# Performance work log

Measured on AMD Instinct MI355X. Metric: run time of the kernel, lower is better.

The kernel has to match this reference:

```python
import jax, jax.numpy as jnp
import numpy as np

NUM_WINDOWS = 162   # icosphere order-2 windows
NUM_HEADS = 8

def layernorm(x, g, b, eps=1e-5):
    m = jnp.mean(x, axis=-1, keepdims=True)
    v = jnp.var(x, axis=-1, keepdims=True)
    return (x - m) * jax.lax.rsqrt(v + eps) * g + b

def setup_inputs() -> dict:
    key = jax.random.key(0)
    ks = jax.random.split(key, 16)
    B, N, C = 1, 41472, 512
    H, hid = NUM_HEADS, 4 * 512
    s = 0.02
    # window assignment: 162 windows x 256 vertices, shuffled (gather-based partition)
    rng = np.random.default_rng(0)
    wid = np.repeat(np.arange(NUM_WINDOWS), N // NUM_WINDOWS)
    rng.shuffle(wid)
    return {
        "x": jax.random.normal(ks[0], (B, N, C), jnp.float32),
        "mesh": jax.random.normal(ks[1], (N, 3), jnp.float32),
        "ln1_g": jnp.ones((C,), jnp.float32),
        "ln1_b": jnp.zeros((C,), jnp.float32),
        "qkv_w": jax.random.normal(ks[2], (C, 3 * C), jnp.float32) * s,
        "qkv_b": jnp.zeros((3 * C,), jnp.float32),
        "rel_bias": jax.random.normal(ks[3], (H, 1, 1), jnp.float32) * s,
        "proj_w": jax.random.normal(ks[4], (C, C), jnp.float32) * s,
        "proj_b": jnp.zeros((C,), jnp.float32),
        "ln2_g": jnp.ones((C,), jnp.float32),
        "ln2_b": jnp.zeros((C,), jnp.float32),
        "ffn_w1": jax.random.normal(ks[5], (C, hid), jnp.float32) * s,
        "ffn_b1": jnp.zeros((hid,), jnp.float32),
        "ffn_w2": jax.random.normal(ks[6], (hid, C), jnp.float32) * s,
        "ffn_b2": jnp.zeros((C,), jnp.float32),
        "window_ids": jnp.asarray(wid, dtype=jnp.int32),
    }

def reference(x, mesh, ln1_g, ln1_b, qkv_w, qkv_b, rel_bias, proj_w, proj_b,
              ln2_g, ln2_b, ffn_w1, ffn_b1, ffn_w2, ffn_b2, window_ids):
    B, N, C = x.shape
    H = NUM_HEADS
    hd = C // H
    ws = N // NUM_WINDOWS
    # --- gather-based window partition ---
    idx = jnp.argsort(window_ids)                      # [N]
    w = x[:, idx, :].reshape(B * NUM_WINDOWS, ws, C)   # [BW, ws, C]
    # --- window attention on norm1(windows) ---
    h = layernorm(w, ln1_g, ln1_b)
    qkv = (h @ qkv_w + qkv_b).reshape(B * NUM_WINDOWS, ws, 3, H, hd)
    q, k, v = qkv[:, :, 0], qkv[:, :, 1], qkv[:, :, 2]  # [BW, ws, H, hd]
    scale = hd ** -0.5
    attn = jnp.einsum('wqhd,wkhd->whqk', q, k) * scale + rel_bias
    attn = jax.nn.softmax(attn, axis=-1)
    out = jnp.einsum('whqk,wkhd->wqhd', attn, v).reshape(B * NUM_WINDOWS, ws, C)
    out = out @ proj_w + proj_b
    # --- reverse partition + residual ---
    inv = jnp.argsort(idx)
    x = x + out.reshape(B, N, C)[:, inv, :]
    # --- FFN block ---
    h2 = layernorm(x, ln2_g, ln2_b)
    f = jax.nn.gelu(h2 @ ffn_w1 + ffn_b1, approximate=False) @ ffn_w2 + ffn_b2
    x = x + f
    return (x, mesh)
```

## Files before the change

### kernel.cpp

```cpp
#include <hip/hip_runtime.h>
#include <hip/hip_bf16.h>
#include <math.h>

#define NW   162
#define WS   256
#define NH   8
#define HD   64
#define CC   512
#define NTOK 41472
#define HID  2048

typedef __bf16 bf16x8 __attribute__((ext_vector_type(8)));
typedef float  floatx4 __attribute__((ext_vector_type(4)));

__device__ __forceinline__ void gload_lds16(const __bf16* g, __bf16* l) {
    __builtin_amdgcn_global_load_lds((const __attribute__((address_space(1))) void*)g,
                                     (__attribute__((address_space(3))) void*)l,
                                     16, 0, 0);
}
__device__ __forceinline__ float fast_rcp(float x) { return __builtin_amdgcn_rcpf(x); }

#define GBAR()  __builtin_amdgcn_s_barrier()
#define VMW(N)  asm volatile("s_waitcnt vmcnt(" #N ")" ::: "memory")
#define LGKM0() asm volatile("s_waitcnt lgkmcnt(0)" ::: "memory")
#define SCHED0() __builtin_amdgcn_sched_barrier(0)

__global__ __launch_bounds__(256)
void build_perm_atomic(const int* __restrict__ wid, int* __restrict__ perm,
                       int* __restrict__ counters) {
    const int i = blockIdx.x * 256 + threadIdx.x;
    const int w = wid[i];
    const int r = atomicAdd(&counters[w], 1);
    perm[w * WS + r] = i;
}

__global__ void transpose_bf16(const float* __restrict__ in,
                               __bf16* __restrict__ out, int K, int N) {
    int idx = blockIdx.x * 256 + threadIdx.x;
    if (idx >= K * N) return;
    int n = idx / K, k = idx - n * K;
    out[idx] = (__bf16)in[(size_t)k * N + n];
}

__global__ __launch_bounds__(64)
void ln1_gather(const float* __restrict__ x, const int* __restrict__ perm,
                const float* __restrict__ g, const float* __restrict__ b,
                __bf16* __restrict__ h) {
    const int j = blockIdx.x, lane = threadIdx.x;
    const int orig = perm[j];
    const float4* xp = (const float4*)(x + (size_t)orig * CC);
    float4 a0 = xp[lane * 2 + 0], a1 = xp[lane * 2 + 1];
    float s  = a0.x + a0.y + a0.z + a0.w + a1.x + a1.y + a1.z + a1.w;
    float sq = a0.x*a0.x + a0.y*a0.y + a0.z*a0.z + a0.w*a0.w
             + a1.x*a1.x + a1.y*a1.y + a1.z*a1.z + a1.w*a1.w;
#pragma unroll
    for (int o = 32; o; o >>= 1) { s += __shfl_xor(s, o); sq += __shfl_xor(sq, o); }
    const float m  = s * (1.f / CC);
    const float rs = rsqrtf(sq * (1.f / CC) - m * m + 1e-5f);
    const float4* g4 = (const float4*)g;  const float4* b4 = (const float4*)b;
    float4 g0 = g4[lane*2+0], g1 = g4[lane*2+1], bb0 = b4[lane*2+0], bb1 = b4[lane*2+1];
    bf16x8 o8;
    o8[0] = (__bf16)((a0.x - m) * rs * g0.x + bb0.x);
    o8[1] = (__bf16)((a0.y - m) * rs * g0.y + bb0.y);
    o8[2] = (__bf16)((a0.z - m) * rs * g0.z + bb0.z);
    o8[3] = (__bf16)((a0.w - m) * rs * g0.w + bb0.w);
    o8[4] = (__bf16)((a1.x - m) * rs * g1.x + bb1.x);
    o8[5] = (__bf16)((a1.y - m) * rs * g1.y + bb1.y);
    o8[6] = (__bf16)((a1.z - m) * rs * g1.z + bb1.z);
    o8[7] = (__bf16)((a1.w - m) * rs * g1.w + bb1.w);
    *(bf16x8*)(h + (size_t)j * CC + lane * 8) = o8;
}

__global__ __launch_bounds__(64)
void ln2_only(const float* __restrict__ x, const float* __restrict__ g,
              const float* __restrict__ b, __bf16* __restrict__ h2) {
    const int i = blockIdx.x, lane = threadIdx.x;
    const float4* xp = (const float4*)(x + (size_t)i * CC);
    float4 a0 = xp[lane*2+0], a1 = xp[lane*2+1];
    float s  = a0.x + a0.y + a0.z + a0.w + a1.x + a1.y + a1.z + a1.w;
    float sq = a0.x*a0.x + a0.y*a0.y + a0.z*a0.z + a0.w*a0.w
             + a1.x*a1.x + a1.y*a1.y + a1.z*a1.z + a1.w*a1.w;
#pragma unroll
    for (int o = 32; o; o >>= 1) { s += __shfl_xor(s, o); sq += __shfl_xor(sq, o); }
    const float m  = s * (1.f / CC);
    const float rs = rsqrtf(sq * (1.f / CC) - m * m + 1e-5f);
    const float4* g4 = (const float4*)g;  const float4* b4 = (const float4*)b;
    float4 g0 = g4[lane*2+0], g1 = g4[lane*2+1], bb0 = b4[lane*2+0], bb1 = b4[lane*2+1];
    bf16x8 o8;
    o8[0] = (__bf16)((a0.x - m) * rs * g0.x + bb0.x);
    o8[1] = (__bf16)((a0.y - m) * rs * g0.y + bb0.y);
    o8[2] = (__bf16)((a0.z - m) * rs * g0.z + bb0.z);
    o8[3] = (__bf16)((a0.w - m) * rs * g0.w + bb0.w);
    o8[4] = (__bf16)((a1.x - m) * rs * g1.x + bb1.x);
    o8[5] = (__bf16)((a1.y - m) * rs * g1.y + bb1.y);
    o8[6] = (__bf16)((a1.z - m) * rs * g1.z + bb1.z);
    o8[7] = (__bf16)((a1.w - m) * rs * g1.w + bb1.w);
    *(bf16x8*)(h2 + (size_t)i * CC + lane * 8) = o8;
}

__device__ __forceinline__ void stage_A(const __bf16* __restrict__ g, int K, int kcol,
                                        __bf16* lds, int h, int tid, int wave) {
    const int sch = ((tid & 7) ^ ((tid >> 3) & 7)) << 3;
#pragma unroll
    for (int j = 0; j < 2; j++) {
        const int rw   = (j * 512 + tid) >> 3;
        const int row  = (rw & 63) + ((rw & 64) << 1) + (h << 6);
        const int rw0  = j * 64 + wave * 8;
        const int row0 = (rw0 & 63) + ((rw0 & 64) << 1) + (h << 6);
        gload_lds16(g + (size_t)row * K + kcol + sch, lds + row0 * 64);
    }
}
__device__ __forceinline__ void stage_B(const __bf16* __restrict__ g, int K, int kcol,
                                        __bf16* lds, int h, int tid, int wave) {
    const int sch = ((tid & 7) ^ ((tid >> 3) & 7)) << 3;
#pragma unroll
    for (int j = 0; j < 2; j++) {
        const int rw   = (j * 512 + tid) >> 3;
        const int row  = (rw & 31) + ((rw >> 5) << 6) + (h << 5);
        const int rw0  = j * 64 + wave * 8;
        const int row0 = (rw0 & 31) + ((rw0 >> 5) << 6) + (h << 5);
        gload_lds16(g + (size_t)row * K + kcol + sch, lds + row0 * 64);
    }
}

__device__ __forceinline__ void load_afr(const __bf16* buf, int wm, int mh,
                                         int lr, int lq, bf16x8 (&af)[4][2]) {
#pragma unroll
    for (int mt = 0; mt < 4; mt++) {
        const __bf16* rp = buf + (wm * 128 + mh * 64 + mt * 16 + lr) * 64;
#pragma unroll
        for (int kk = 0; kk < 2; kk++)
            af[mt][kk] = *(const bf16x8*)(rp + (((kk * 4 + lq) ^ (lr & 7)) << 3));
    }
}
__device__ __forceinline__ void load_bfr(const __bf16* buf, int wn, int nh,
                                         int lr, int lq, bf16x8 (&bf)[2][2]) {
#pragma unroll
    for (int nt = 0; nt < 2; nt++) {
        const __bf16* rp = buf + (wn * 64 + nh * 32 + nt * 16 + lr) * 64;
#pragma unroll
        for (int kk = 0; kk < 2; kk++)
            bf[nt][kk] = *(const bf16x8*)(rp + (((kk * 4 + lq) ^ (lr & 7)) << 3));
    }
}

#define MFMA_QUAD(MH, NH, AF, BF)                                              \
    _Pragma("unroll") for (int kk_ = 0; kk_ < 2; kk_++)                        \
    _Pragma("unroll") for (int mt_ = 0; mt_ < 4; mt_++)                        \
    _Pragma("unroll") for (int nt_ = 0; nt_ < 2; nt_++)                        \
        acc[(MH) * 4 + mt_][(NH) * 2 + nt_] =                                  \
            __builtin_amdgcn_mfma_f32_16x16x32_bf16(                           \
                AF[mt_][kk_], BF[nt_][kk_],                                    \
                acc[(MH) * 4 + mt_][(NH) * 2 + nt_], 0, 0, 0);

template <int EPI>
__device__ __forceinline__
void gemm_body(const __bf16* __restrict__ A, const __bf16* __restrict__ Bt,
               const float* __restrict__ bias, const float* __restrict__ res,
               float* __restrict__ Cf, __bf16* __restrict__ Cb,
               int M, int N, int K, const int* __restrict__ prm) {
    __shared__ __bf16 smem[65536];
    __bf16* Ac = smem;
    __bf16* An = smem + 16384;
    __bf16* Bc = smem + 32768;
    __bf16* Bn = smem + 49152;

    const int tid  = threadIdx.x;
    const int wave = tid >> 6;
    const int lane = tid & 63;
    const int wm = wave >> 2, wn = wave & 3;
    const int lr = lane & 15, lq = lane >> 4;

    const int gx  = gridDim.x;
    const int nwg = gx * gridDim.y;
    const int orig = blockIdx.y * gx + blockIdx.x;
    const int q8 = nwg >> 3, r8 = nwg & 7;
    const int xcd = orig & 7, oi = orig >> 3;
    const int wgid = (xcd < r8 ? xcd * (q8 + 1) : r8 * (q8 + 1) + (xcd - r8) * q8) + oi;
    const int bm = wgid / gx, bn = wgid - bm * gx;

    const __bf16* gA = A  + (size_t)bm * 256 * K;
    const __bf16* gB = Bt + (size_t)bn * 256 * K;
    const int NT = K >> 6;

    floatx4 acc[8][4];
#pragma unroll
    for (int i = 0; i < 8; i++)
#pragma unroll
        for (int j = 0; j < 4; j++) acc[i][j] = (floatx4){0.f, 0.f, 0.f, 0.f};

    stage_A(gA, K, 0, Ac, 0, tid, wave);
    stage_B(gB, K, 0, Bc, 0, tid, wave);
    stage_B(gB, K, 0, Bc, 1, tid, wave);
    stage_A(gA, K, 0, Ac, 1, tid, wave);
    if (NT > 1) stage_A(gA, K, 64, An, 0, tid, wave);
    VMW(4);
    GBAR();

    bf16x8 af[4][2], b0[2][2], b1[2][2];

    for (int t = 0; t < NT; t++) {
        const int k1 = (t + 1) << 6;
        if (t == NT - 1) { VMW(0); } else { VMW(4); }
        if (t + 1 < NT) stage_B(gB, K, k1, Bn, 0, tid, wave);
        load_afr(Ac, wm, 0, lr, lq, af);
        load_bfr(Bc, wn, 0, lr, lq, b0);
        GBAR(); LGKM0(); SCHED0();
        __builtin_amdgcn_s_setprio(1);
        MFMA_QUAD(0, 0, af, b0);
        __builtin_amdgcn_s_setprio(0);
        VMW(4);
        if (t + 1 < NT) stage_B(gB, K, k1, Bn, 1, tid, wave);
        load_bfr(Bc, wn, 1, lr, lq, b1);
        GBAR(); LGKM0(); SCHED0();
        __builtin_amdgcn_s_setprio(1);
        MFMA_QUAD(0, 1, af, b1);
        __builtin_amdgcn_s_setprio(0);
        VMW(4);
        if (t + 1 < NT) stage_A(gA, K, k1, An, 1, tid, wave);
        load_afr(Ac, wm, 1, lr, lq, af);
        GBAR(); LGKM0(); SCHED0();
        __builtin_amdgcn_s_setprio(1);
        MFMA_QUAD(1, 1, af, b1);
        __builtin_amdgcn_s_setprio(0);
        VMW(4);
        if (t + 2 < NT) stage_A(gA, K, (t + 2) << 6, Ac, 0, tid, wave);
        GBAR();
        __builtin_amdgcn_s_setprio(1);
        MFMA_QUAD(1, 0, af, b0);
        __builtin_amdgcn_s_setprio(0);
        __bf16* ta = Ac; Ac = An; An = ta;
        __bf16* tb = Bc; Bc = Bn; Bn = tb;
    }

    if constexpr (EPI == 0 || EPI == 2) {
        GBAR();
        __bf16* Ct = smem;
#pragma unroll
        for (int m = 0; m < 8; m++)
#pragma unroll
            for (int n = 0; n < 4; n++) {
                const int col = wn * 64 + n * 16 + lr;
                const float bv = bias[bn * 256 + col];
#pragma unroll
                for (int r = 0; r < 4; r++) {
                    float v = acc[m][n][r] + bv;
                    if constexpr (EPI == 2) {
                        const float e = __expf(v * -1.702f);
                        v = v * fast_rcp(1.f + e);
                    }
                    Ct[(wm * 128 + m * 16 + lq * 4 + r) * 256 + col] = (__bf16)v;
                }
            }
        __syncthreads();
#pragma unroll
        for (int j = 0; j < 16; j++) {
            const int ci = j * 512 + tid;
            const int row = ci >> 5, ch = ci & 31;
            *(bf16x8*)(Cb + (size_t)(bm * 256 + row) * N + bn * 256 + ch * 8) =
                *(const bf16x8*)(Ct + row * 256 + ch * 8);
        }
    } else {
#pragma unroll
        for (int m = 0; m < 8; m++) {
            const int row = bm * 256 + wm * 128 + m * 16 + lq * 4;
            int tok[4];
            if constexpr (EPI == 4) {
#pragma unroll
                for (int r = 0; r < 4; r++) tok[r] = prm[row + r];
            }
#pragma unroll
            for (int n = 0; n < 4; n++) {
                const int col = bn * 256 + wn * 64 + n * 16 + lr;
                const float bv = bias[col];
#pragma unroll
                for (int r = 0; r < 4; r++) {
                    const float v = acc[m][n][r] + bv;
                    if constexpr (EPI == 1) {
                        Cf[(size_t)(row + r) * N + col] = v;
                    } else if constexpr (EPI == 3) {
                        const size_t off = (size_t)(row + r) * N + col;
                        Cf[off] = res[off] + v;
                    } else {
                        const size_t off = (size_t)tok[r] * N + col;
                        Cf[off] = res[off] + v;
                    }
                }
            }
        }
    }
}

__global__ __launch_bounds__(512, 2)
void gemm_qkv(const __bf16* __restrict__ A, const __bf16* __restrict__ Bt,
              const float* __restrict__ bias, __bf16* __restrict__ Cb, int N, int K) {
    gemm_body<0>(A, Bt, bias, nullptr, nullptr, Cb, NTOK, N, K, nullptr);
}
__global__ __launch_bounds__(512, 2)
void gemm_proj(const __bf16* __restrict__ A, const __bf16* __restrict__ Bt,
               const float* __restrict__ bias, const float* __restrict__ res,
               float* __restrict__ Cf, const int* __restrict__ prm, int N, int K) {
    gemm_body<4>(A, Bt, bias, res, Cf, nullptr, NTOK, N, K, prm);
}
__global__ __launch_bounds__(512, 2)
void gemm_ffn1(const __bf16* __restrict__ A, const __bf16* __restrict__ Bt,
               const float* __restrict__ bias, __bf16* __restrict__ Cb, int N, int K) {
    gemm_body<2>(A, Bt, bias, nullptr, nullptr, Cb, NTOK, N, K, nullptr);
}
__global__ __launch_bounds__(512, 2)
void gemm_ffn2(const __bf16* __restrict__ A, const __bf16* __restrict__ Bt,
               const float* __restrict__ bias, const float* __restrict__ res,
               float* __restrict__ Cf, int N, int K) {
    gemm_body<3>(A, Bt, bias, res, Cf, nullptr, NTOK, N, K, nullptr);
}

__global__ __launch_bounds__(256)
void attn_mfma(const __bf16* __restrict__ qkv, __bf16* __restrict__ aout,
               const float* __restrict__ rel_bias) {
    __shared__ __bf16 vsT[HD * WS];
    __shared__ __bf16 pbuf[4][64][34];
    const int w = blockIdx.x, h = blockIdx.y;
    const int tid = threadIdx.x;
    const int wave = tid >> 6, lane = tid & 63;
    const int lr = lane & 15, lq = lane >> 4;
    const size_t base = (size_t)w * (WS * 1536) + h * 64;

    for (int c = tid; c < WS * 8; c += 256) {
        const int key = c >> 3, d8 = c & 7;
        bf16x8 vv = *(const bf16x8*)(qkv + base + 1024 + (size_t)key * 1536 + d8 * 8);
#pragma unroll
        for (int jj = 0; jj < 8; jj++) {
            const int d = d8 * 8 + jj;
            vsT[d * WS + (((key >> 3) ^ (d & 31)) << 3) + (key & 7)] = vv[jj];
        }
    }

    const int q0 = wave * 64;
    bf16x8 qf[4][2];
#pragma unroll
    for (int mt = 0; mt < 4; mt++)
#pragma unroll
        for (int kk = 0; kk < 2; kk++)
            qf[mt][kk] = *(const bf16x8*)(qkv + base +
                (size_t)(q0 + mt * 16 + lr) * 1536 + kk * 32 + lq * 8);

    __syncthreads();

    floatx4 o[4][4];
    float lsum[4][4];
#pragma unroll
    for (int mt = 0; mt < 4; mt++)
#pragma unroll
        for (int dt = 0; dt < 4; dt++) o[mt][dt] = (floatx4){0.f, 0.f, 0.f, 0.f};
#pragma unroll
    for (int mt = 0; mt < 4; mt++)
#pragma unroll
        for (int r = 0; r < 4; r++) lsum[mt][r] = 0.f;

    const float sc = 0.125f * 1.44269504089f;
    const float bb = rel_bias[h] * 1.44269504089f;
    const __bf16* kp0 = qkv + base + 512;

    bf16x8 kc[2][2];
#pragma unroll
    for (int nt = 0; nt < 2; nt++) {
        const __bf16* kp = kp0 + (size_t)(nt * 16 + lr) * 1536 + lq * 8;
        kc[nt][0] = *(const bf16x8*)(kp);
        kc[nt][1] = *(const bf16x8*)(kp + 32);
    }

    for (int kt = 0; kt < 8; kt++) {
        const int kbase = kt * 32;
        bf16x8 kn[2][2];
        if (kt < 7) {
#pragma unroll
            for (int nt = 0; nt < 2; nt++) {
                const __bf16* kp = kp0 + (size_t)(kbase + 32 + nt * 16 + lr) * 1536 + lq * 8;
                kn[nt][0] = *(const bf16x8*)(kp);
                kn[nt][1] = *(const bf16x8*)(kp + 32);
            }
        }
        floatx4 s[4][2];
#pragma unroll
        for (int mt = 0; mt < 4; mt++)
#pragma unroll
            for (int nt = 0; nt < 2; nt++) s[mt][nt] = (floatx4){0.f, 0.f, 0.f, 0.f};
#pragma unroll
        for (int nt = 0; nt < 2; nt++)
#pragma unroll
            for (int mt = 0; mt < 4; mt++) {
                s[mt][nt] = __builtin_amdgcn_mfma_f32_16x16x32_bf16(qf[mt][0], kc[nt][0], s[mt][nt], 0, 0, 0);
                s[mt][nt] = __builtin_amdgcn_mfma_f32_16x16x32_bf16(qf[mt][1], kc[nt][1], s[mt][nt], 0, 0, 0);
            }
#pragma unroll
        for (int mt = 0; mt < 4; mt++)
#pragma unroll
            for (int nt = 0; nt < 2; nt++)
#pragma unroll
                for (int r = 0; r < 4; r++) {
                    float e = exp2f(s[mt][nt][r] * sc + bb);
                    lsum[mt][r] += e;
                    pbuf[wave][mt * 16 + lq * 4 + r][nt * 16 + lr] = (__bf16)e;
                }
        bf16x8 vf[4];
#pragma unroll
        for (int dt = 0; dt < 4; dt++) {
            const int d = dt * 16 + lr;
            vf[dt] = *(const bf16x8*)(vsT + d * WS +
                                      (((kt * 4 + lq) ^ (d & 31)) << 3));
        }
#pragma unroll
        for (int mt = 0; mt < 4; mt++) {
            bf16x8 pf = *(const bf16x8*)(&pbuf[wave][mt * 16 + lr][lq * 8]);
#pragma unroll
            for (int dt = 0; dt < 4; dt++)
                o[mt][dt] = __builtin_amdgcn_mfma_f32_16x16x32_bf16(pf, vf[dt], o[mt][dt], 0, 0, 0);
        }
#pragma unroll
        for (int nt = 0; nt < 2; nt++) { kc[nt][0] = kn[nt][0]; kc[nt][1] = kn[nt][1]; }
    }

#pragma unroll
    for (int mt = 0; mt < 4; mt++)
#pragma unroll
        for (int r = 0; r < 4; r++) {
            float v = lsum[mt][r];
            v += __shfl_xor(v, 1); v += __shfl_xor(v, 2);
            v += __shfl_xor(v, 4); v += __shfl_xor(v, 8);
            lsum[mt][r] = fast_rcp(v);
        }

#pragma unroll
    for (int dh = 0; dh < 2; dh++) {
#pragma unroll
        for (int mt = 0; mt < 4; mt++)
#pragma unroll
            for (int dt = 0; dt < 2; dt++)
#pragma unroll
                for (int r = 0; r < 4; r++)
                    pbuf[wave][mt * 16 + lq * 4 + r][dt * 16 + lr] =
                        (__bf16)(o[mt][dh * 2 + dt][r] * lsum[mt][r]);
#pragma unroll
        for (int it = 0; it < 4; it++) {
            const int c = it * 64 + lane;
            const int row = c >> 2, seg = c & 3;
            bf16x8 val = *(const bf16x8*)(&pbuf[wave][row][seg * 8]);
            *(bf16x8*)(aout + (size_t)(w * WS + q0 + row) * CC + h * 64 + dh * 32 + seg * 8) = val;
        }
    }
}

extern "C" void kernel_launch(void* const* d_in, const int* in_sizes, int n_in,
                              void* d_out, int out_size, void* d_ws, size_t ws_size,
                              hipStream_t stream) {
    const float* x      = (const float*)d_in[0];
    const float* mesh   = (const float*)d_in[1];
    const float* ln1_g  = (const float*)d_in[2];
    const float* ln1_b  = (const float*)d_in[3];
    const float* qkv_w  = (const float*)d_in[4];
    const float* qkv_b  = (const float*)d_in[5];
    const float* rel_b  = (const float*)d_in[6];
    const float* proj_w = (const float*)d_in[7];
    const float* proj_b = (const float*)d_in[8];
    const float* ln2_g  = (const float*)d_in[9];
    const float* ln2_b  = (const float*)d_in[10];
    const float* w1     = (const float*)d_in[11];
    const float* b1     = (const float*)d_in[12];
    const float* w2     = (const float*)d_in[13];
    const float* b2     = (const float*)d_in[14];
    const int*   wid    = (const int*)d_in[15];

    char* ws = (char*)d_ws;
    int*    perm  = (int*)(ws + 0);
    __bf16* wqkv  = (__bf16*)(ws + 331776);
    __bf16* wproj = (__bf16*)(ws + 1904640);
    __bf16* w1t   = (__bf16*)(ws + 2428928);
    __bf16* w2t   = (__bf16*)(ws + 4526080);
    const size_t BB = 6623232;
    __bf16* hln1 = (__bf16*)(ws + BB);
    __bf16* qkv  = (__bf16*)(ws + BB + 42467328);
    __bf16* aout = (__bf16*)(ws + BB + 169869312);
    __bf16* h2   = (__bf16*)(ws + BB + 84934656);
    __bf16* f1   = (__bf16*)(ws + BB + 127401984);
    float*  xout = (float*)d_out;
    int*    counters = (int*)aout;

    hipMemsetAsync(counters, 0, NW * sizeof(int), stream);
    build_perm_atomic<<<NTOK / 256, 256, 0, stream>>>(wid, perm, counters);

    transpose_bf16<<<(512 * 1536 + 255) / 256, 256, 0, stream>>>(qkv_w, wqkv, 512, 1536);
    transpose_bf16<<<(512 * 512 + 255) / 256, 256, 0, stream>>>(proj_w, wproj, 512, 512);
    transpose_bf16<<<(512 * 2048 + 255) / 256, 256, 0, stream>>>(w1, w1t, 512, 2048);
    transpose_bf16<<<(2048 * 512 + 255) / 256, 256, 0, stream>>>(w2, w2t, 2048, 512);

    ln1_gather<<<NTOK, 64, 0, stream>>>(x, perm, ln1_g, ln1_b, hln1);

    gemm_qkv<<<dim3(1536 / 256, NTOK / 256), 512, 0, stream>>>(
        hln1, wqkv, qkv_b, qkv, 1536, 512);

    attn_mfma<<<dim3(NW, NH), 256, 0, stream>>>(qkv, aout, rel_b);

    gemm_proj<<<dim3(512 / 256, NTOK / 256), 512, 0, stream>>>(
        aout, wproj, proj_b, x, xout, perm, 512, 512);

    ln2_only<<<NTOK, 64, 0, stream>>>(xout, ln2_g, ln2_b, h2);

    gemm_ffn1<<<dim3(2048 / 256, NTOK / 256), 512, 0, stream>>>(
        h2, w1t, b1, f1, 2048, 512);

    gemm_ffn2<<<dim3(512 / 256, NTOK / 256), 512, 0, stream>>>(
        f1, w2t, b2, xout, xout, 512, 2048);

    hipMemcpyAsync((char*)d_out + (size_t)NTOK * CC * 4, mesh,
                   (size_t)NTOK * 3 * 4, hipMemcpyDeviceToDevice, stream);
}
```

Baseline: 727.3 us.

## Load GEMM B operand directly from global into register double buffers

```diff
diff --git a/kernel.cpp b/kernel.cpp
--- a/kernel.cpp
+++ b/kernel.cpp
@@ -110,18 +110,6 @@
         gload_lds16(g + (size_t)row * K + kcol + sch, lds + row0 * 64);
     }
 }
-__device__ __forceinline__ void stage_B(const __bf16* __restrict__ g, int K, int kcol,
-                                        __bf16* lds, int h, int tid, int wave) {
-    const int sch = ((tid & 7) ^ ((tid >> 3) & 7)) << 3;
-#pragma unroll
-    for (int j = 0; j < 2; j++) {
-        const int rw   = (j * 512 + tid) >> 3;
-        const int row  = (rw & 31) + ((rw >> 5) << 6) + (h << 5);
-        const int rw0  = j * 64 + wave * 8;
-        const int row0 = (rw0 & 31) + ((rw0 >> 5) << 6) + (h << 5);
-        gload_lds16(g + (size_t)row * K + kcol + sch, lds + row0 * 64);
-    }
-}
 
 __device__ __forceinline__ void load_afr(const __bf16* buf, int wm, int mh,
                                          int lr, int lq, bf16x8 (&af)[4][2]) {
@@ -133,14 +121,15 @@
             af[mt][kk] = *(const bf16x8*)(rp + (((kk * 4 + lq) ^ (lr & 7)) << 3));
     }
 }
-__device__ __forceinline__ void load_bfr(const __bf16* buf, int wn, int nh,
-                                         int lr, int lq, bf16x8 (&bf)[2][2]) {
+
+__device__ __forceinline__ void loadB_g(const __bf16* __restrict__ gBw, int K, int kcol,
+                                        int nh, int lr, int lq, bf16x8 (&bf)[2][2]) {
 #pragma unroll
     for (int nt = 0; nt < 2; nt++) {
-        const __bf16* rp = buf + (wn * 64 + nh * 32 + nt * 16 + lr) * 64;
+        const __bf16* rp = gBw + (size_t)(nh * 32 + nt * 16 + lr) * K + kcol + lq * 8;
 #pragma unroll
         for (int kk = 0; kk < 2; kk++)
-            bf[nt][kk] = *(const bf16x8*)(rp + (((kk * 4 + lq) ^ (lr & 7)) << 3));
+            bf[nt][kk] = *(const bf16x8*)(rp + kk * 32);
     }
 }
 
@@ -162,8 +151,6 @@
     __shared__ __bf16 smem[65536];
     __bf16* Ac = smem;
     __bf16* An = smem + 16384;
-    __bf16* Bc = smem + 32768;
-    __bf16* Bn = smem + 49152;
 
     const int tid  = threadIdx.x;
     const int wave = tid >> 6;
@@ -179,8 +166,8 @@
     const int wgid = (xcd < r8 ? xcd * (q8 + 1) : r8 * (q8 + 1) + (xcd - r8) * q8) + oi;
     const int bm = wgid / gx, bn = wgid - bm * gx;
 
-    const __bf16* gA = A  + (size_t)bm * 256 * K;
-    const __bf16* gB = Bt + (size_t)bn * 256 * K;
+    const __bf16* gA  = A  + (size_t)bm * 256 * K;
+    const __bf16* gBw = Bt + (size_t)(bn * 256 + wn * 64) * K;
     const int NT = K >> 6;
 
     floatx4 acc[8][4];
@@ -189,48 +176,51 @@
 #pragma unroll
         for (int j = 0; j < 4; j++) acc[i][j] = (floatx4){0.f, 0.f, 0.f, 0.f};
 
+    bf16x8 af[4][2];
+    bf16x8 bc0[2][2], bc1[2][2], bn0[2][2], bn1[2][2];
+
     stage_A(gA, K, 0, Ac, 0, tid, wave);
-    stage_B(gB, K, 0, Bc, 0, tid, wave);
-    stage_B(gB, K, 0, Bc, 1, tid, wave);
+    loadB_g(gBw, K, 0, 0, lr, lq, bc0);
+    loadB_g(gBw, K, 0, 1, lr, lq, bc1);
     stage_A(gA, K, 0, Ac, 1, tid, wave);
     if (NT > 1) stage_A(gA, K, 64, An, 0, tid, wave);
-    VMW(4);
-    GBAR();
-
-    bf16x8 af[4][2], b0[2][2], b1[2][2];
-
-    for (int t = 0; t < NT; t++) {
+
+    auto tile_step = [&](int t, bf16x8 (&c0)[2][2], bf16x8 (&c1)[2][2],
+                         bf16x8 (&n0)[2][2], bf16x8 (&n1)[2][2]) {
         const int k1 = (t + 1) << 6;
-        if (t == NT - 1) { VMW(0); } else { VMW(4); }
-        if (t + 1 < NT) stage_B(gB, K, k1, Bn, 0, tid, wave);
+        const bool s = (t + 1 < NT);
+        if (s) { VMW(8); } else { VMW(6); }
+        if (s) loadB_g(gBw, K, k1, 0, lr, lq, n0);
+        GBAR();
         load_afr(Ac, wm, 0, lr, lq, af);
-        load_bfr(Bc, wn, 0, lr, lq, b0);
-        GBAR(); LGKM0(); SCHED0();
+        LGKM0(); SCHED0();
         __builtin_amdgcn_s_setprio(1);
-        MFMA_QUAD(0, 0, af, b0);
+        MFMA_QUAD(0, 0, af, c0);
         __builtin_amdgcn_s_setprio(0);
-        VMW(4);
-        if (t + 1 < NT) stage_B(gB, K, k1, Bn, 1, tid, wave);
-        load_bfr(Bc, wn, 1, lr, lq, b1);
-        GBAR(); LGKM0(); SCHED0();
+        if (s) { VMW(8); } else { VMW(2); }
+        if (s) loadB_g(gBw, K, k1, 1, lr, lq, n1);
+        SCHED0();
         __builtin_amdgcn_s_setprio(1);
-        MFMA_QUAD(0, 1, af, b1);
+        MFMA_QUAD(0, 1, af, c1);
         __builtin_amdgcn_s_setprio(0);
-        VMW(4);
-        if (t + 1 < NT) stage_A(gA, K, k1, An, 1, tid, wave);
+        if (s) { VMW(10); } else { VMW(0); }
+        if (s) stage_A(gA, K, k1, An, 1, tid, wave);
+        GBAR();
         load_afr(Ac, wm, 1, lr, lq, af);
-        GBAR(); LGKM0(); SCHED0();
+        LGKM0(); SCHED0();
         __builtin_amdgcn_s_setprio(1);
-        MFMA_QUAD(1, 1, af, b1);
+        MFMA_QUAD(1, 1, af, c1);
         __builtin_amdgcn_s_setprio(0);
-        VMW(4);
         if (t + 2 < NT) stage_A(gA, K, (t + 2) << 6, Ac, 0, tid, wave);
-        GBAR();
         __builtin_amdgcn_s_setprio(1);
-        MFMA_QUAD(1, 0, af, b0);
+        MFMA_QUAD(1, 0, af, c0);
         __builtin_amdgcn_s_setprio(0);
         __bf16* ta = Ac; Ac = An; An = ta;
-        __bf16* tb = Bc; Bc = Bn; Bn = tb;
+    };
+
+    for (int t = 0; t < NT; t += 2) {
+        tile_step(t,     bc0, bc1, bn0, bn1);
+        tile_step(t + 1, bn0, bn1, bc0, bc1);
     }
 
     if constexpr (EPI == 0 || EPI == 2) {
```

After: 1.097 ms. 50.9% more time.

## Use 128x256 tile GEMM kernel for N=512 proj and FFN2 layers

Applied to the files above, without the earlier changes.

```diff
diff --git a/kernel.cpp b/kernel.cpp
--- a/kernel.cpp
+++ b/kernel.cpp
@@ -110,6 +110,16 @@
         gload_lds16(g + (size_t)row * K + kcol + sch, lds + row0 * 64);
     }
 }
+__device__ __forceinline__ void stage_A128(const __bf16* __restrict__ g, int K, int kcol,
+                                           __bf16* lds, int tid, int wave) {
+    const int sch = ((tid & 7) ^ ((tid >> 3) & 7)) << 3;
+#pragma unroll
+    for (int j = 0; j < 2; j++) {
+        const int row  = (j * 512 + tid) >> 3;
+        const int row0 = j * 64 + wave * 8;
+        gload_lds16(g + (size_t)row * K + kcol + sch, lds + row0 * 64);
+    }
+}
 __device__ __forceinline__ void stage_B(const __bf16* __restrict__ g, int K, int kcol,
                                         __bf16* lds, int h, int tid, int wave) {
     const int sch = ((tid & 7) ^ ((tid >> 3) & 7)) << 3;
@@ -128,6 +138,16 @@
 #pragma unroll
     for (int mt = 0; mt < 4; mt++) {
         const __bf16* rp = buf + (wm * 128 + mh * 64 + mt * 16 + lr) * 64;
+#pragma unroll
+        for (int kk = 0; kk < 2; kk++)
+            af[mt][kk] = *(const bf16x8*)(rp + (((kk * 4 + lq) ^ (lr & 7)) << 3));
+    }
+}
+__device__ __forceinline__ void load_afr64(const __bf16* buf, int wm,
+                                           int lr, int lq, bf16x8 (&af)[4][2]) {
+#pragma unroll
+    for (int mt = 0; mt < 4; mt++) {
+        const __bf16* rp = buf + (wm * 64 + mt * 16 + lr) * 64;
 #pragma unroll
         for (int kk = 0; kk < 2; kk++)
             af[mt][kk] = *(const bf16x8*)(rp + (((kk * 4 + lq) ^ (lr & 7)) << 3));
@@ -153,12 +173,20 @@
                 AF[mt_][kk_], BF[nt_][kk_],                                    \
                 acc[(MH) * 4 + mt_][(NH) * 2 + nt_], 0, 0, 0);
 
+#define MFMA_Q128(NH, AF, BF)                                                  \
+    _Pragma("unroll") for (int kk_ = 0; kk_ < 2; kk_++)                        \
+    _Pragma("unroll") for (int mt_ = 0; mt_ < 4; mt_++)                        \
+    _Pragma("unroll") for (int nt_ = 0; nt_ < 2; nt_++)                        \
+        acc[mt_][(NH) * 2 + nt_] =                                             \
+            __builtin_amdgcn_mfma_f32_16x16x32_bf16(                           \
+                AF[mt_][kk_], BF[nt_][kk_],                                    \
+                acc[mt_][(NH) * 2 + nt_], 0, 0, 0);
+
 template <int EPI>
 __device__ __forceinline__
 void gemm_body(const __bf16* __restrict__ A, const __bf16* __restrict__ Bt,
-               const float* __restrict__ bias, const float* __restrict__ res,
-               float* __restrict__ Cf, __bf16* __restrict__ Cb,
-               int M, int N, int K, const int* __restrict__ prm) {
+               const float* __restrict__ bias, __bf16* __restrict__ Cb,
+               int M, int N, int K) {
     __shared__ __bf16 smem[65536];
     __bf16* Ac = smem;
     __bf16* An = smem + 16384;
@@ -233,58 +261,123 @@
         __bf16* tb = Bc; Bc = Bn; Bn = tb;
     }
 
-    if constexpr (EPI == 0 || EPI == 2) {
+    GBAR();
+    __bf16* Ct = smem;
+#pragma unroll
+    for (int m = 0; m < 8; m++)
+#pragma unroll
+        for (int n = 0; n < 4; n++) {
+            const int col = wn * 64 + n * 16 + lr;
+            const float bv = bias[bn * 256 + col];
+#pragma unroll
+            for (int r = 0; r < 4; r++) {
+                float v = acc[m][n][r] + bv;
+                if constexpr (EPI == 2) {
+                    const float e = __expf(v * -1.702f);
+                    v = v * fast_rcp(1.f + e);
+                }
+                Ct[(wm * 128 + m * 16 + lq * 4 + r) * 256 + col] = (__bf16)v;
+            }
+        }
+    __syncthreads();
+#pragma unroll
+    for (int j = 0; j < 16; j++) {
+        const int ci = j * 512 + tid;
+        const int row = ci >> 5, ch = ci & 31;
+        *(bf16x8*)(Cb + (size_t)(bm * 256 + row) * N + bn * 256 + ch * 8) =
+            *(const bf16x8*)(Ct + row * 256 + ch * 8);
+    }
+}
+
+template <int EPI>
+__device__ __forceinline__
+void gemm_body128(const __bf16* __restrict__ A, const __bf16* __restrict__ Bt,
+                  const float* __restrict__ bias, const float* __restrict__ res,
+                  float* __restrict__ Cf, int M, int N, int K,
+                  const int* __restrict__ prm) {
+    __shared__ __bf16 smem[49152];
+    __bf16* Ac = smem;
+    __bf16* An = smem + 8192;
+    __bf16* Bc = smem + 16384;
+    __bf16* Bn = smem + 32768;
+
+    const int tid  = threadIdx.x;
+    const int wave = tid >> 6;
+    const int lane = tid & 63;
+    const int wm = wave >> 2, wn = wave & 3;
+    const int lr = lane & 15, lq = lane >> 4;
+
+    const int gx  = gridDim.x;
+    const int nwg = gx * gridDim.y;
+    const int orig = blockIdx.y * gx + blockIdx.x;
+    const int q8 = nwg >> 3, r8 = nwg & 7;
+    const int xcd = orig & 7, oi = orig >> 3;
+    const int wgid = (xcd < r8 ? xcd * (q8 + 1) : r8 * (q8 + 1) + (xcd - r8) * q8) + oi;
+    const int bm = wgid / gx, bn = wgid - bm * gx;
+
+    const __bf16* gA = A  + (size_t)bm * 128 * K;
+    const __bf16* gB = Bt + (size_t)bn * 256 * K;
+    const int NT = K >> 6;
+
+    floatx4 acc[4][4];
+#pragma unroll
+    for (int i = 0; i < 4; i++)
+#pragma unroll
+        for (int j = 0; j < 4; j++) acc[i][j] = (floatx4){0.f, 0.f, 0.f, 0.f};
+
+    stage_A128(gA, K, 0, Ac, tid, wave);
+    stage_B(gB, K, 0, Bc, 0, tid, wave);
+    stage_B(gB, K, 0, Bc, 1, tid, wave);
+
+    bf16x8 af[4][2], b0[2][2], b1[2][2];
+
+    for (int t = 0; t < NT; t++) {
+        const int k1 = (t + 1) << 6;
+        VMW(2);
+        if (t + 1 < NT) stage_A128(gA, K, k1, An, tid, wave);
         GBAR();
-        __bf16* Ct = smem;
-#pragma unroll
-        for (int m = 0; m < 8; m++)
-#pragma unroll
-            for (int n = 0; n < 4; n++) {
-                const int col = wn * 64 + n * 16 + lr;
-                const float bv = bias[bn * 256 + col];
-#pragma unroll
-                for (int r = 0; r < 4; r++) {
-                    float v = acc[m][n][r] + bv;
-                    if constexpr (EPI == 2) {
-                        const float e = __expf(v * -1.702f);
-                        v = v * fast_rcp(1.f + e);
-                    }
-                    Ct[(wm * 128 + m * 16 + lq * 4 + r) * 256 + col] = (__bf16)v;
-                }
-            }
-        __syncthreads();
-#pragma unroll
-        for (int j = 0; j < 16; j++) {
-            const int ci = j * 512 + tid;
-            const int row = ci >> 5, ch = ci & 31;
-            *(bf16x8*)(Cb + (size_t)(bm * 256 + row) * N + bn * 256 + ch * 8) =
-                *(const bf16x8*)(Ct + row * 256 + ch * 8);
-        }
-    } else {
-#pragma unroll
-        for (int m = 0; m < 8; m++) {
-            const int row = bm * 256 + wm * 128 + m * 16 + lq * 4;
-            int tok[4];
-            if constexpr (EPI == 4) {
-#pragma unroll
-                for (int r = 0; r < 4; r++) tok[r] = prm[row + r];
-            }
-#pragma unroll
-            for (int n = 0; n < 4; n++) {
-                const int col = bn * 256 + wn * 64 + n * 16 + lr;
-                const float bv = bias[col];
-#pragma unroll
-                for (int r = 0; r < 4; r++) {
-                    const float v = acc[m][n][r] + bv;
-                    if constexpr (EPI == 1) {
-                        Cf[(size_t)(row + r) * N + col] = v;
-                    } else if constexpr (EPI == 3) {
-                        const size_t off = (size_t)(row + r) * N + col;
-                        Cf[off] = res[off] + v;
-                    } else {
-                        const size_t off = (size_t)tok[r] * N + col;
-                        Cf[off] = res[off] + v;
-                    }
+        load_afr64(Ac, wm, lr, lq, af);
+        load_bfr(Bc, wn, 0, lr, lq, b0);
+        LGKM0(); SCHED0();
+        __builtin_amdgcn_s_setprio(1);
+        MFMA_Q128(0, af, b0);
+        __builtin_amdgcn_s_setprio(0);
+        if (t == NT - 1) { VMW(0); } else { VMW(2); }
+        if (t + 1 < NT) {
+            stage_B(gB, K, k1, Bn, 0, tid, wave);
+            stage_B(gB, K, k1, Bn, 1, tid, wave);
+        }
+        GBAR();
+        load_bfr(Bc, wn, 1, lr, lq, b1);
+        LGKM0(); SCHED0();
+        __builtin_amdgcn_s_setprio(1);
+        MFMA_Q128(1, af, b1);
+        __builtin_amdgcn_s_setprio(0);
+        __bf16* ta = Ac; Ac = An; An = ta;
+        __bf16* tb = Bc; Bc = Bn; Bn = tb;
+    }
+
+#pragma unroll
+    for (int m = 0; m < 4; m++) {
+        const int row = bm * 128 + wm * 64 + m * 16 + lq * 4;
+        int tok[4];
+        if constexpr (EPI == 4) {
+#pragma unroll
+            for (int r = 0; r < 4; r++) tok[r] = prm[row + r];
+        }
+#pragma unroll
+        for (int n = 0; n < 4; n++) {
+            const int col = bn * 256 + wn * 64 + n * 16 + lr;
+            const float bv = bias[col];
+#pragma unroll
+            for (int r = 0; r < 4; r++) {
+                const float v = acc[m][n][r] + bv;
+                if constexpr (EPI == 3) {
+                    const size_t off = (size_t)(row + r) * N + col;
+                    Cf[off] = res[off] + v;
+                } else {
+                    const size_t off = (size_t)tok[r] * N + col;
+                    Cf[off] = res[off] + v;
                 }
             }
         }
@@ -294,24 +387,24 @@
 __global__ __launch_bounds__(512, 2)
 void gemm_qkv(const __bf16* __restrict__ A, const __bf16* __restrict__ Bt,
               const float* __restrict__ bias, __bf16* __restrict__ Cb, int N, int K) {
-    gemm_body<0>(A, Bt, bias, nullptr, nullptr, Cb, NTOK, N, K, nullptr);
+    gemm_body<0>(A, Bt, bias, Cb, NTOK, N, K);
+}
+__global__ __launch_bounds__(512, 2)
+void gemm_ffn1(const __bf16* __restrict__ A, const __bf16* __restrict__ Bt,
+               const float* __restrict__ bias, __bf16* __restrict__ Cb, int N, int K) {
+    gemm_body<2>(A, Bt, bias, Cb, NTOK, N, K);
 }
 __global__ __launch_bounds__(512, 2)
 void gemm_proj(const __bf16* __restrict__ A, const __bf16* __restrict__ Bt,
                const float* __restrict__ bias, const float* __restrict__ res,
                float* __restrict__ Cf, const int* __restrict__ prm, int N, int K) {
-    gemm_body<4>(A, Bt, bias, res, Cf, nullptr, NTOK, N, K, prm);
-}
-__global__ __launch_bounds__(512, 2)
-void gemm_ffn1(const __bf16* __restrict__ A, const __bf16* __restrict__ Bt,
-               const float* __restrict__ bias, __bf16* __restrict__ Cb, int N, int K) {
-    gemm_body<2>(A, Bt, bias, nullptr, nullptr, Cb, NTOK, N, K, nullptr);
+    gemm_body128<4>(A, Bt, bias, res, Cf, NTOK, N, K, prm);
 }
 __global__ __launch_bounds__(512, 2)
 void gemm_ffn2(const __bf16* __restrict__ A, const __bf16* __restrict__ Bt,
                const float* __restrict__ bias, const float* __restrict__ res,
                float* __restrict__ Cf, int N, int K) {
-    gemm_body<3>(A, Bt, bias, res, Cf, nullptr, NTOK, N, K, nullptr);
+    gemm_body128<3>(A, Bt, bias, res, Cf, NTOK, N, K, nullptr);
 }
 
 __global__ __launch_bounds__(256)
@@ -500,7 +593,7 @@
 
     attn_mfma<<<dim3(NW, NH), 256, 0, stream>>>(qkv, aout, rel_b);
 
-    gemm_proj<<<dim3(512 / 256, NTOK / 256), 512, 0, stream>>>(
+    gemm_proj<<<dim3(512 / 256, NTOK / 128), 512, 0, stream>>>(
         aout, wproj, proj_b, x, xout, perm, 512, 512);
 
     ln2_only<<<NTOK, 64, 0, stream>>>(xout, ln2_g, ln2_b, h2);
@@ -508,7 +601,7 @@
     gemm_ffn1<<<dim3(2048 / 256, NTOK / 256), 512, 0, stream>>>(
         h2, w1t, b1, f1, 2048, 512);
 
-    gemm_ffn2<<<dim3(512 / 256, NTOK / 256), 512, 0, stream>>>(
+    gemm_ffn2<<<dim3(512 / 256, NTOK / 128), 512, 0, stream>>>(
         f1, w2t, b2, xout, xout, 512, 2048);
 
     hipMemcpyAsync((char*)d_out + (size_t)NTOK * CC * 4, mesh,
```

New measurement: 716.2 us. No clear change (-1.5%).
